# Kernel optimization log

Measured on AMD Instinct MI355X. Metric: run time of the kernel, lower is better.

## Reference

```python
import jax, jax.numpy as jnp
import numpy as np

DIM = 1024
NUM_HEADS = 16
HEAD_DIM = DIM // NUM_HEADS
ROPE_BASE = 10000.0


def _rope_cos_sin(seq_len, head_dim, dtype):
    # inv_freq over even indices of head_dim
    inv_freq = 1.0 / (ROPE_BASE ** (jnp.arange(0, head_dim, 2, dtype=jnp.float32) / head_dim))
    t = jnp.arange(seq_len, dtype=jnp.float32)
    freqs = jnp.einsum('i,j->ij', t, inv_freq)        # [N, D/2]
    emb = jnp.concatenate([freqs, freqs], axis=-1)    # [N, D]
    return jnp.cos(emb).astype(dtype), jnp.sin(emb).astype(dtype)


def _rotate_half(x):
    x1, x2 = jnp.split(x, 2, axis=-1)
    return jnp.concatenate([-x2, x1], axis=-1)


def setup_inputs() -> dict:
    key = jax.random.key(0)
    k1, k2, k3 = jax.random.split(key, 3)
    B, N = 2, 2048
    x = jax.random.normal(k1, (B, N, DIM), dtype=jnp.float32)
    # torch Linear weights: [out_features, in_features]; init scale ~1/sqrt(dim)
    Wqkv = jax.random.normal(k2, (3 * DIM, DIM), dtype=jnp.float32) * (DIM ** -0.5)
    Wproj = jax.random.normal(k3, (DIM, DIM), dtype=jnp.float32) * (DIM ** -0.5)
    return {"x": x, "Wqkv": Wqkv, "Wproj": Wproj}


def reference(x, Wqkv, Wproj):
    B, N, C = x.shape
    H, D = NUM_HEADS, HEAD_DIM
    # QKV projection: [B,N,3C] -> [3,B,H,N,D]
    qkv = jnp.einsum('bnc,oc->bno', x, Wqkv)
    qkv = qkv.reshape(B, N, 3, H, D).transpose(2, 0, 3, 1, 4)
    q, k, v = qkv[0], qkv[1], qkv[2]                  # each [B,H,N,D]
    # RoPE
    cos, sin = _rope_cos_sin(N, D, x.dtype)           # [N,D] each
    cos = cos[None, None, :, :]
    sin = sin[None, None, :, :]
    q = q * cos + _rotate_half(q) * sin
    k = k * cos + _rotate_half(k) * sin
    # scaled dot-product attention (non-causal, no mask, no dropout)
    scale = 1.0 / jnp.sqrt(jnp.asarray(D, dtype=x.dtype))
    scores = jnp.einsum('bhnd,bhmd->bhnm', q, k) * scale
    attn = jax.nn.softmax(scores, axis=-1)
    out = jnp.einsum('bhnm,bhmd->bhnd', attn, v)      # [B,H,N,D]
    out = out.transpose(0, 2, 1, 3).reshape(B, N, C)
    return jnp.einsum('bnc,oc->bno', out, Wproj)
```

## Files before the change

### kernel.cpp

```cpp
#include <hip/hip_runtime.h>
#include <hip/hip_bf16.h>

#define SEQ   2048
#define DIMC  1024
#define NH    16
#define HD    64
#define QKV3  3072
#define NB    2
#define SCALE_LOG2E 0.18033688011112042f
#define SM_BIAS 16.0f

typedef __attribute__((ext_vector_type(8)))  short bf16x8;
typedef __attribute__((ext_vector_type(4)))  float f32x4;
typedef __attribute__((ext_vector_type(16))) float f32x16;

__device__ __forceinline__ unsigned short f2bf(float f){
  union { float f; unsigned int u; } v; v.f = f;
  return (unsigned short)((v.u + 0x7fffu + ((v.u >> 16) & 1u)) >> 16);
}
__device__ __forceinline__ float bf2f(unsigned short h){
  union { unsigned int u; float f; } v; v.u = ((unsigned int)h) << 16; return v.f;
}
__device__ __forceinline__ int packbf2(float a, float b){
  __hip_bfloat162 h = __float22bfloat162_rn(make_float2(a, b));
  int r; __builtin_memcpy(&r, &h, 4); return r;
}
__device__ __forceinline__ void async_lds16(void* lds, const void* g){
  __builtin_amdgcn_global_load_lds(
      (const __attribute__((address_space(1))) void*)g,
      (__attribute__((address_space(3))) void*)lds, 16, 0, 0);
}

__global__ __launch_bounds__(256) void k_prep(const float* __restrict__ x,
                                              const float* __restrict__ wqkv,
                                              const float* __restrict__ wproj,
                                              unsigned short* __restrict__ xb,
                                              unsigned short* __restrict__ wqkvb,
                                              unsigned short* __restrict__ wprojb,
                                              float2* __restrict__ tab){
  const int b = blockIdx.x, tid = threadIdx.x;
  if (b < 8192){
    const float* in; unsigned short* out; int i;
    if (b < 4096)      { in = x;     out = xb;     i = b * 256 + tid; }
    else if (b < 7168) { in = wqkv;  out = wqkvb;  i = (b - 4096) * 256 + tid; }
    else               { in = wproj; out = wprojb; i = (b - 7168) * 256 + tid; }
    const float4 v = ((const float4*)in)[i];
    union { unsigned short s[4]; unsigned long long u; } p;
    p.s[0] = f2bf(v.x); p.s[1] = f2bf(v.y); p.s[2] = f2bf(v.z); p.s[3] = f2bf(v.w);
    *(unsigned long long*)(out + (size_t)i * 4) = p.u;
  } else {
    const int idx = (b - 8192) * 256 + tid;
    const int n = idx >> 5, j = idx & 31;
    const float inv = 1.0f / powf(10000.0f, (float)(2 * j) * (1.0f / 64.0f));
    const float f = (float)n * inv;
    tab[idx] = make_float2(cosf(f), sinf(f));
  }
}

template<int OUT_BF16, int BM, int BN>
__global__ __launch_bounds__(256) void k_gemm(const unsigned short* __restrict__ A,
                                              const unsigned short* __restrict__ Bm,
                                              void* __restrict__ Cp, int M, int N, int K){
  constexpr int FM = BM / 32, FN = BN / 32;
  constexpr int CA = BM / 32, CB = BN / 32;
  __shared__ unsigned short As[BM * 64];
  __shared__ unsigned short Bs[BN * 64];
  const int tid = threadIdx.x, wave = tid >> 6, lane = tid & 63;
  const int nbn = N / BN;
  const int bm = blockIdx.x / nbn, bn = blockIdx.x % nbn;
  const int m0 = bm * BM, n0 = bn * BN;
  const int wr = wave >> 1, wc = wave & 1;

  f32x4 acc[FM][FN];
#pragma unroll
  for (int i = 0; i < FM; i++)
#pragma unroll
    for (int j = 0; j < FN; j++) acc[i][j] = (f32x4){0.f, 0.f, 0.f, 0.f};

  for (int k0 = 0; k0 < K; k0 += 64){
#pragma unroll
    for (int c = 0; c < CA; c++){
      const int e = c * 2048 + tid * 8;
      const int row = e >> 6, col = e & 63;
      async_lds16(As + c * 2048 + wave * 512, A + (size_t)(m0 + row) * K + k0 + col);
    }
#pragma unroll
    for (int c = 0; c < CB; c++){
      const int e = c * 2048 + tid * 8;
      const int row = e >> 6, col = e & 63;
      async_lds16(Bs + c * 2048 + wave * 512, Bm + (size_t)(n0 + row) * K + k0 + col);
    }
    __syncthreads();
#pragma unroll
    for (int ks = 0; ks < 2; ks++){
      const int kk = ks * 32 + (lane >> 4) * 8;
      bf16x8 af[FM], bfr[FN];
#pragma unroll
      for (int i = 0; i < FM; i++)
        af[i]  = *(const bf16x8*)&As[(wr * (BM / 2) + i * 16 + (lane & 15)) * 64 + kk];
#pragma unroll
      for (int j = 0; j < FN; j++)
        bfr[j] = *(const bf16x8*)&Bs[(wc * (BN / 2) + j * 16 + (lane & 15)) * 64 + kk];
#pragma unroll
      for (int i = 0; i < FM; i++)
#pragma unroll
        for (int j = 0; j < FN; j++)
          acc[i][j] = __builtin_amdgcn_mfma_f32_16x16x32_bf16(af[i], bfr[j], acc[i][j], 0, 0, 0);
    }
    __syncthreads();
  }
#pragma unroll
  for (int i = 0; i < FM; i++)
#pragma unroll
    for (int j = 0; j < FN; j++)
#pragma unroll
      for (int r = 0; r < 4; r++){
        const int row = m0 + wr * (BM / 2) + i * 16 + (lane >> 4) * 4 + r;
        const int col = n0 + wc * (BN / 2) + j * 16 + (lane & 15);
        const float v = acc[i][j][r];
        if constexpr (OUT_BF16) ((unsigned short*)Cp)[(size_t)row * N + col] = f2bf(v);
        else                    ((float*)Cp)[(size_t)row * N + col] = v;
      }
}

__global__ __launch_bounds__(256) void k_post(const unsigned short* __restrict__ qkv,
                                              const float2* __restrict__ tab,
                                              unsigned short* __restrict__ Qb,
                                              unsigned short* __restrict__ Kswz,
                                              unsigned short* __restrict__ Vt){
  __shared__ unsigned short t[64 * 72];
  if (blockIdx.x < 2048){
    unsigned int idx = blockIdx.x * 256 + threadIdx.x;
    const int j = idx & 3; idx >>= 2;
    const int n = idx & 2047; idx >>= 11;
    const int h = idx & 15; idx >>= 4;
    const int b = idx & 1;
    const int which = idx >> 1;
    const size_t rowbase = ((size_t)(b * SEQ + n)) * QKV3 + which * DIMC + h * HD;
    const bf16x8 lo = *(const bf16x8*)&qkv[rowbase + j * 8];
    const bf16x8 hi = *(const bf16x8*)&qkv[rowbase + 32 + j * 8];
    union { unsigned short s[8]; bf16x8 v; } olo, ohi;
#pragma unroll
    for (int u = 0; u < 8; u++){
      const float2 cs = tab[n * 32 + j * 8 + u];
      const float xl = bf2f((unsigned short)lo[u]), xh = bf2f((unsigned short)hi[u]);
      float yl = xl * cs.x - xh * cs.y;
      float yh = xh * cs.x + xl * cs.y;
      if (which == 0){ yl *= SCALE_LOG2E; yh *= SCALE_LOG2E; }
      olo.s[u] = f2bf(yl); ohi.s[u] = f2bf(yh);
    }
    if (which == 0){
      const size_t orow = (((size_t)(b * NH + h)) * SEQ + n) * HD;
      *(bf16x8*)&Qb[orow + j * 8]      = olo.v;
      *(bf16x8*)&Qb[orow + 32 + j * 8] = ohi.v;
    } else {
      const int np = (n & ~31) | (n & 0x13) | ((n & 4) << 1) | ((n & 8) >> 1);
      const int s = (np & 7) << 3;
      const size_t orow = (((size_t)(b * NH + h)) * SEQ + np) * HD;
      *(bf16x8*)&Kswz[orow + ((j * 8) ^ s)]      = olo.v;
      *(bf16x8*)&Kswz[orow + ((32 + j * 8) ^ s)] = ohi.v;
    }
  } else {
    const int i2 = blockIdx.x - 2048, tid = threadIdx.x;
    const int nt = i2 & 31, h = (i2 >> 5) & 15, b = i2 >> 9;
    const int n0 = nt * 64;
#pragma unroll
    for (int p = 0; p < 2; p++){
      const int e = p * 2048 + tid * 8;
      const int r = e >> 6, c = e & 63;
      *(bf16x8*)&t[r * 72 + c] =
          *(const bf16x8*)&qkv[((size_t)(b * SEQ + n0 + r)) * QKV3 + 2048 + h * 64 + c];
    }
    __syncthreads();
#pragma unroll
    for (int p = 0; p < 2; p++){
      const int e = p * 2048 + tid * 8;
      const int d = e >> 6, nn = e & 63;
      const int sw = (d & 7) << 3;
      union { unsigned short s[8]; bf16x8 v; } o;
#pragma unroll
      for (int q = 0; q < 8; q++) o.s[q] = t[((nn ^ sw) + q) * 72 + d];
      *(bf16x8*)&Vt[(((size_t)(b * NH + h)) * HD + d) * SEQ + n0 + nn] = o.v;
    }
  }
}

__global__ __launch_bounds__(256) void k_attn(const unsigned short* __restrict__ Q,
                                              const unsigned short* __restrict__ Kg,
                                              const unsigned short* __restrict__ Vg,
                                              unsigned short* __restrict__ AO){
  __shared__ unsigned short Ks[2][128 * 64];
  __shared__ unsigned short Vs[2][64 * 128];
  const int tid = threadIdx.x, wave = tid >> 6, lane = tid & 63;
  const int bh = blockIdx.x & 31, qt = blockIdx.x >> 5;
  const size_t base = (size_t)bh * (SEQ * HD);
  const int q32 = lane & 31, hi = lane >> 5, hi8 = hi << 3;
  const int sw = (q32 & 7) << 3;
  const int q0w = qt * 128 + wave * 32;

  bf16x8 qf[4];
#pragma unroll
  for (int kc = 0; kc < 4; kc++)
    qf[kc] = *(const bf16x8*)&Q[base + (size_t)(q0w + q32) * HD + kc * 16 + hi8];

  f32x16 oacc[2];
#pragma unroll
  for (int md = 0; md < 2; md++)
#pragma unroll
    for (int r = 0; r < 16; r++) oacc[md][r] = 0.f;
  float lrow = 0.f;

  const int krow = wave * 8 + (lane >> 3), kcol = (lane & 7) * 8;
  const int vd   = wave * 4 + (lane >> 4), vcol = (lane & 15) * 8;

  auto stage = [&](int buf, int kv0){
#pragma unroll
    for (int r = 0; r < 4; r++)
      async_lds16(&Ks[buf][r * 2048 + wave * 512],
                  &Kg[base + (size_t)(kv0 + r * 32 + krow) * HD + kcol]);
#pragma unroll
    for (int r = 0; r < 4; r++)
      async_lds16(&Vs[buf][r * 2048 + wave * 512],
                  &Vg[base + (size_t)(r * 16 + vd) * SEQ + kv0 + vcol]);
  };

  stage(0, 0);
  asm volatile("s_waitcnt vmcnt(0)" ::: "memory");
  __syncthreads();

#pragma unroll 1
  for (int t = 0; t < 16; t++){
    const int cur = t & 1;
    if (t < 15) stage(cur ^ 1, (t + 1) * 128);

    f32x16 s[4];
#pragma unroll
    for (int k2 = 0; k2 < 4; k2++)
#pragma unroll
      for (int r = 0; r < 16; r++) s[k2][r] = -SM_BIAS;
    __builtin_amdgcn_s_setprio(1);
#pragma unroll
    for (int k2 = 0; k2 < 4; k2++)
#pragma unroll
      for (int kc = 0; kc < 4; kc++){
        const bf16x8 kf = *(const bf16x8*)&Ks[cur][(k2 * 32 + q32) * 64 + ((kc * 16 + hi8) ^ sw)];
        s[k2] = __builtin_amdgcn_mfma_f32_32x32x16_bf16(kf, qf[kc], s[k2], 0, 0, 0);
      }
    __builtin_amdgcn_s_setprio(0);

#pragma unroll
    for (int k2 = 0; k2 < 4; k2++)
#pragma unroll
      for (int r = 0; r < 16; r++)
        s[k2][r] = __builtin_amdgcn_exp2f(s[k2][r]);
    float a16[16];
#pragma unroll
    for (int r = 0; r < 16; r++)
      a16[r] = (s[0][r] + s[1][r]) + (s[2][r] + s[3][r]);
#pragma unroll
    for (int r = 0; r < 8; r++) a16[r] += a16[r + 8];
    float rs = ((a16[0] + a16[1]) + (a16[2] + a16[3])) + ((a16[4] + a16[5]) + (a16[6] + a16[7]));
    rs += __shfl_xor(rs, 32);
    lrow += rs;

    __builtin_amdgcn_s_setprio(1);
#pragma unroll
    for (int g2 = 0; g2 < 8; g2++){
      const int k2 = g2 >> 1, off = (g2 & 1) * 8;
      union { int w[4]; bf16x8 v; } pb;
      pb.w[0] = packbf2(s[k2][off + 0], s[k2][off + 1]);
      pb.w[1] = packbf2(s[k2][off + 2], s[k2][off + 3]);
      pb.w[2] = packbf2(s[k2][off + 4], s[k2][off + 5]);
      pb.w[3] = packbf2(s[k2][off + 6], s[k2][off + 7]);
      const int col = g2 * 16 + hi8;
      const int colA = ((col & 63) ^ sw) | (col & 64);
#pragma unroll
      for (int md = 0; md < 2; md++){
        const bf16x8 av = *(const bf16x8*)&Vs[cur][(md * 32 + q32) * 128 + colA];
        oacc[md] = __builtin_amdgcn_mfma_f32_32x32x16_bf16(av, pb.v, oacc[md], 0, 0, 0);
      }
    }
    __builtin_amdgcn_s_setprio(0);

    asm volatile("s_waitcnt vmcnt(0)" ::: "memory");
    __syncthreads();
  }

  const float rl = 1.0f / lrow;
  const int b = bh >> 4, h = bh & 15;
  const size_t obase = ((size_t)(b * SEQ + q0w + q32)) * DIMC + h * HD;
#pragma unroll
  for (int md = 0; md < 2; md++)
#pragma unroll
    for (int a = 0; a < 4; a++){
      const int d0 = md * 32 + a * 8 + hi * 4;
      int2 wv;
      wv.x = packbf2(oacc[md][a * 4 + 0] * rl, oacc[md][a * 4 + 1] * rl);
      wv.y = packbf2(oacc[md][a * 4 + 2] * rl, oacc[md][a * 4 + 3] * rl);
      *(int2*)&AO[obase + d0] = wv;
    }
}

extern "C" void kernel_launch(void* const* d_in, const int* in_sizes, int n_in,
                              void* d_out, int out_size, void* d_ws, size_t ws_size,
                              hipStream_t stream){
  const float* x     = (const float*)d_in[0];
  const float* Wqkv  = (const float*)d_in[1];
  const float* Wproj = (const float*)d_in[2];
  float* out = (float*)d_out;
  char* ws = (char*)d_ws;

  unsigned short* xb     = (unsigned short*)(ws);
  unsigned short* wqkvb  = (unsigned short*)(ws +  8388608);
  unsigned short* wprojb = (unsigned short*)(ws + 14680064);
  unsigned short* qkvb   = (unsigned short*)(ws + 16777216);
  float2*         tab    = (float2*)        (ws + 41943040);
  unsigned short* Qb     = (unsigned short*)(ws + 42467328);
  unsigned short* Kb     = (unsigned short*)(ws + 50855936);
  unsigned short* Vtb    = (unsigned short*)(ws + 59244544);
  unsigned short* AOb    = (unsigned short*)(ws);

  k_prep<<<8448, 256, 0, stream>>>(x, Wqkv, Wproj, xb, wqkvb, wprojb, tab);
  k_gemm<1, 128, 128><<<768, 256, 0, stream>>>(xb, wqkvb, (void*)qkvb, 4096, 3072, 1024);
  k_post<<<3072, 256, 0, stream>>>(qkvb, tab, Qb, Kb, Vtb);
  k_attn<<<512, 256, 0, stream>>>(Qb, Kb, Vtb, AOb);
  k_gemm<0, 64, 128><<<512, 256, 0, stream>>>(AOb, wprojb, (void*)out, 4096, 1024, 1024);
}
```

Baseline: 205.3 us.

## Fuse RoPE, Q scaling and K swizzle into QKV GEMM epilogue

```diff
diff --git a/kernel.cpp b/kernel.cpp
--- a/kernel.cpp
+++ b/kernel.cpp
@@ -5,7 +5,6 @@
 #define DIMC  1024
 #define NH    16
 #define HD    64
-#define QKV3  3072
 #define NB    2
 #define SCALE_LOG2E 0.18033688011112042f
 #define SM_BIAS 16.0f
@@ -57,6 +56,101 @@
   }
 }
 
+__global__ __launch_bounds__(256) void k_gemmqkv(const unsigned short* __restrict__ A,
+                                                 const unsigned short* __restrict__ Bm,
+                                                 const float2* __restrict__ tab,
+                                                 unsigned short* __restrict__ Qb,
+                                                 unsigned short* __restrict__ Kswz,
+                                                 unsigned short* __restrict__ vbuf){
+  constexpr int K = 1024, N = 3072;
+  __shared__ unsigned short As[128 * 64];
+  __shared__ unsigned short Bs[128 * 64];
+  const int tid = threadIdx.x, wave = tid >> 6, lane = tid & 63;
+  const int bm = blockIdx.x / 24, bn = blockIdx.x % 24;
+  const int m0 = bm << 7, n0 = bn << 7;
+  const int wr = wave >> 1, wc = wave & 1;
+
+  f32x4 acc[4][4];
+#pragma unroll
+  for (int i = 0; i < 4; i++)
+#pragma unroll
+    for (int j = 0; j < 4; j++) acc[i][j] = (f32x4){0.f, 0.f, 0.f, 0.f};
+
+  for (int k0 = 0; k0 < K; k0 += 64){
+#pragma unroll
+    for (int c = 0; c < 4; c++){
+      const int e = c * 2048 + tid * 8;
+      const int row = e >> 6, col = e & 63;
+      async_lds16(As + c * 2048 + wave * 512, A + (size_t)(m0 + row) * K + k0 + col);
+      async_lds16(Bs + c * 2048 + wave * 512, Bm + (size_t)(n0 + row) * K + k0 + col);
+    }
+    __syncthreads();
+#pragma unroll
+    for (int ks = 0; ks < 2; ks++){
+      const int kk = ks * 32 + (lane >> 4) * 8;
+      bf16x8 af[4], bfr[4];
+#pragma unroll
+      for (int i = 0; i < 4; i++){
+        af[i]  = *(const bf16x8*)&As[(wr * 64 + i * 16 + (lane & 15)) * 64 + kk];
+        bfr[i] = *(const bf16x8*)&Bs[(wc * 64 + i * 16 + (lane & 15)) * 64 + kk];
+      }
+#pragma unroll
+      for (int i = 0; i < 4; i++)
+#pragma unroll
+        for (int j = 0; j < 4; j++)
+          acc[i][j] = __builtin_amdgcn_mfma_f32_16x16x32_bf16(af[i], bfr[j], acc[i][j], 0, 0, 0);
+    }
+    __syncthreads();
+  }
+
+  const int l15 = lane & 15;
+  const int which = bn >> 3;
+  if (which == 2){
+#pragma unroll
+    for (int i = 0; i < 4; i++)
+#pragma unroll
+      for (int j = 0; j < 4; j++)
+#pragma unroll
+        for (int r = 0; r < 4; r++){
+          const int row = m0 + wr * 64 + i * 16 + (lane >> 4) * 4 + r;
+          const int col = (bn & 7) * 128 + wc * 64 + j * 16 + l15;
+          vbuf[(size_t)row * 1024 + col] = f2bf(acc[i][j][r]);
+        }
+  } else {
+    const int h = (bn & 7) * 2 + wc;
+#pragma unroll
+    for (int i = 0; i < 4; i++)
+#pragma unroll
+      for (int r = 0; r < 4; r++){
+        const int row = m0 + wr * 64 + i * 16 + (lane >> 4) * 4 + r;
+        const int nn = row & 2047, b = row >> 11;
+        const float2 cs0 = tab[nn * 32 + l15];
+        const float2 cs1 = tab[nn * 32 + 16 + l15];
+        const float x0 = acc[i][0][r], x1 = acc[i][1][r];
+        const float x2 = acc[i][2][r], x3 = acc[i][3][r];
+        const float y0 = x0 * cs0.x - x2 * cs0.y;
+        const float y1 = x1 * cs1.x - x3 * cs1.y;
+        const float y2 = x2 * cs0.x + x0 * cs0.y;
+        const float y3 = x3 * cs1.x + x1 * cs1.y;
+        if (which == 0){
+          const size_t orow = ((size_t)(b * NH + h) * SEQ + nn) * HD;
+          Qb[orow + l15]      = f2bf(y0 * SCALE_LOG2E);
+          Qb[orow + 16 + l15] = f2bf(y1 * SCALE_LOG2E);
+          Qb[orow + 32 + l15] = f2bf(y2 * SCALE_LOG2E);
+          Qb[orow + 48 + l15] = f2bf(y3 * SCALE_LOG2E);
+        } else {
+          const int np = (nn & ~31) | (nn & 0x13) | ((nn & 4) << 1) | ((nn & 8) >> 1);
+          const int s = (np & 7) << 3;
+          const size_t orow = ((size_t)(b * NH + h) * SEQ + np) * HD;
+          Kswz[orow + (l15 ^ s)]        = f2bf(y0);
+          Kswz[orow + ((16 + l15) ^ s)] = f2bf(y1);
+          Kswz[orow + ((32 + l15) ^ s)] = f2bf(y2);
+          Kswz[orow + ((48 + l15) ^ s)] = f2bf(y3);
+        }
+      }
+  }
+}
+
 template<int OUT_BF16, int BM, int BN>
 __global__ __launch_bounds__(256) void k_gemm(const unsigned short* __restrict__ A,
                                               const unsigned short* __restrict__ Bm,
@@ -123,65 +217,29 @@
       }
 }
 
-__global__ __launch_bounds__(256) void k_post(const unsigned short* __restrict__ qkv,
-                                              const float2* __restrict__ tab,
-                                              unsigned short* __restrict__ Qb,
-                                              unsigned short* __restrict__ Kswz,
-                                              unsigned short* __restrict__ Vt){
+__global__ __launch_bounds__(256) void k_vt(const unsigned short* __restrict__ vbuf,
+                                            unsigned short* __restrict__ Vt){
   __shared__ unsigned short t[64 * 72];
-  if (blockIdx.x < 2048){
-    unsigned int idx = blockIdx.x * 256 + threadIdx.x;
-    const int j = idx & 3; idx >>= 2;
-    const int n = idx & 2047; idx >>= 11;
-    const int h = idx & 15; idx >>= 4;
-    const int b = idx & 1;
-    const int which = idx >> 1;
-    const size_t rowbase = ((size_t)(b * SEQ + n)) * QKV3 + which * DIMC + h * HD;
-    const bf16x8 lo = *(const bf16x8*)&qkv[rowbase + j * 8];
-    const bf16x8 hi = *(const bf16x8*)&qkv[rowbase + 32 + j * 8];
-    union { unsigned short s[8]; bf16x8 v; } olo, ohi;
-#pragma unroll
-    for (int u = 0; u < 8; u++){
-      const float2 cs = tab[n * 32 + j * 8 + u];
-      const float xl = bf2f((unsigned short)lo[u]), xh = bf2f((unsigned short)hi[u]);
-      float yl = xl * cs.x - xh * cs.y;
-      float yh = xh * cs.x + xl * cs.y;
-      if (which == 0){ yl *= SCALE_LOG2E; yh *= SCALE_LOG2E; }
-      olo.s[u] = f2bf(yl); ohi.s[u] = f2bf(yh);
-    }
-    if (which == 0){
-      const size_t orow = (((size_t)(b * NH + h)) * SEQ + n) * HD;
-      *(bf16x8*)&Qb[orow + j * 8]      = olo.v;
-      *(bf16x8*)&Qb[orow + 32 + j * 8] = ohi.v;
-    } else {
-      const int np = (n & ~31) | (n & 0x13) | ((n & 4) << 1) | ((n & 8) >> 1);
-      const int s = (np & 7) << 3;
-      const size_t orow = (((size_t)(b * NH + h)) * SEQ + np) * HD;
-      *(bf16x8*)&Kswz[orow + ((j * 8) ^ s)]      = olo.v;
-      *(bf16x8*)&Kswz[orow + ((32 + j * 8) ^ s)] = ohi.v;
-    }
-  } else {
-    const int i2 = blockIdx.x - 2048, tid = threadIdx.x;
-    const int nt = i2 & 31, h = (i2 >> 5) & 15, b = i2 >> 9;
-    const int n0 = nt * 64;
-#pragma unroll
-    for (int p = 0; p < 2; p++){
-      const int e = p * 2048 + tid * 8;
-      const int r = e >> 6, c = e & 63;
-      *(bf16x8*)&t[r * 72 + c] =
-          *(const bf16x8*)&qkv[((size_t)(b * SEQ + n0 + r)) * QKV3 + 2048 + h * 64 + c];
-    }
-    __syncthreads();
-#pragma unroll
-    for (int p = 0; p < 2; p++){
-      const int e = p * 2048 + tid * 8;
-      const int d = e >> 6, nn = e & 63;
-      const int sw = (d & 7) << 3;
-      union { unsigned short s[8]; bf16x8 v; } o;
-#pragma unroll
-      for (int q = 0; q < 8; q++) o.s[q] = t[((nn ^ sw) + q) * 72 + d];
-      *(bf16x8*)&Vt[(((size_t)(b * NH + h)) * HD + d) * SEQ + n0 + nn] = o.v;
-    }
+  const int tid = threadIdx.x;
+  const int nt = blockIdx.x & 31, h = (blockIdx.x >> 5) & 15, b = blockIdx.x >> 9;
+  const int n0 = nt * 64;
+#pragma unroll
+  for (int p = 0; p < 2; p++){
+    const int e = p * 2048 + tid * 8;
+    const int r = e >> 6, c = e & 63;
+    *(bf16x8*)&t[r * 72 + c] =
+        *(const bf16x8*)&vbuf[((size_t)(b * SEQ + n0 + r)) * 1024 + h * 64 + c];
+  }
+  __syncthreads();
+#pragma unroll
+  for (int p = 0; p < 2; p++){
+    const int e = p * 2048 + tid * 8;
+    const int d = e >> 6, nn = e & 63;
+    const int sw = (d & 7) << 3;
+    union { unsigned short s[8]; bf16x8 v; } o;
+#pragma unroll
+    for (int q = 0; q < 8; q++) o.s[q] = t[((nn ^ sw) + q) * 72 + d];
+    *(bf16x8*)&Vt[(((size_t)(b * NH + h)) * HD + d) * SEQ + n0 + nn] = o.v;
   }
 }
 
@@ -313,16 +371,16 @@
   unsigned short* xb     = (unsigned short*)(ws);
   unsigned short* wqkvb  = (unsigned short*)(ws +  8388608);
   unsigned short* wprojb = (unsigned short*)(ws + 14680064);
-  unsigned short* qkvb   = (unsigned short*)(ws + 16777216);
-  float2*         tab    = (float2*)        (ws + 41943040);
-  unsigned short* Qb     = (unsigned short*)(ws + 42467328);
-  unsigned short* Kb     = (unsigned short*)(ws + 50855936);
-  unsigned short* Vtb    = (unsigned short*)(ws + 59244544);
+  float2*         tab    = (float2*)        (ws + 16777216);
+  unsigned short* Qb     = (unsigned short*)(ws + 17301504);
+  unsigned short* Kb     = (unsigned short*)(ws + 25690112);
+  unsigned short* vbuf   = (unsigned short*)(ws + 34078720);
+  unsigned short* Vtb    = (unsigned short*)(ws + 42467328);
   unsigned short* AOb    = (unsigned short*)(ws);
 
   k_prep<<<8448, 256, 0, stream>>>(x, Wqkv, Wproj, xb, wqkvb, wprojb, tab);
-  k_gemm<1, 128, 128><<<768, 256, 0, stream>>>(xb, wqkvb, (void*)qkvb, 4096, 3072, 1024);
-  k_post<<<3072, 256, 0, stream>>>(qkvb, tab, Qb, Kb, Vtb);
+  k_gemmqkv<<<768, 256, 0, stream>>>(xb, wqkvb, tab, Qb, Kb, vbuf);
+  k_vt<<<1024, 256, 0, stream>>>(vbuf, Vtb);
   k_attn<<<512, 256, 0, stream>>>(Qb, Kb, Vtb, AOb);
   k_gemm<0, 64, 128><<<512, 256, 0, stream>>>(AOb, wprojb, (void*)out, 4096, 1024, 1024);
 }
```

New measurement: 204.0 us. Within noise of the previous version (-0.6%).
